# Performance work log

Measured on AMD Instinct MI355X. Metric: run time of the kernel, lower is better.

Reference implementation:

```python
import jax, jax.numpy as jnp
import numpy as np

EPS = 1e-6


def setup_inputs() -> dict:
    key = jax.random.key(0)
    k1, k2 = jax.random.split(key)
    T, B, D, n = 2048, 16, 1024, 64
    x = jax.random.normal(k1, (T, B, D), dtype=jnp.float32)
    S0 = jnp.zeros((B, n, n), dtype=jnp.float32)
    G0 = jnp.zeros((B, n, n), dtype=jnp.float32)
    # xavier-uniform-ish init for each n x D block of the fused projection
    limit = float(np.sqrt(6.0 / (n + D)))
    W_kvqm = jax.random.uniform(k2, (4 * n, D), dtype=jnp.float32, minval=-limit, maxval=limit)
    b_s_gate = jnp.full((n,), 2.0, dtype=jnp.float32)
    b_g_gate = jnp.full((n,), 2.5, dtype=jnp.float32)
    return {"x": x, "S0": S0, "G0": G0, "W_kvqm": W_kvqm,
            "b_s_gate": b_s_gate, "b_g_gate": b_g_gate}


def _e81_forward(x, S0, G0, W_kvqm, b_s_gate, b_g_gate):
    T, B, D = x.shape
    n = b_s_gate.shape[0]
    # Fused projection: [T, B, 4n]
    proj = jnp.einsum('tbd,nd->tbn', x, W_kvqm)
    k_all, v_all, q_all, m_all = jnp.split(proj, 4, axis=-1)

    bs = b_s_gate[None, :, None]  # broadcast over [B, n(row), n(col)]
    bg = b_g_gate[None, :, None]

    def step(carry, kvqm):
        S, G = carry
        k, v, q, m_vec = kvqm  # each [B, n]
        k_norm = k / (jnp.linalg.norm(k, axis=-1, keepdims=True) + EPS)
        m_norm = m_vec / (jnp.linalg.norm(m_vec, axis=-1, keepdims=True) + EPS)

        gate_S = jax.nn.sigmoid(G + bs)
        s_retrieved = jnp.einsum('bij,bj->bi', S, k_norm)
        s_delta = v - s_retrieved
        S = gate_S * S + jnp.einsum('bi,bj->bij', s_delta, k_norm)

        gate_G = jax.nn.sigmoid(S + bg)
        g_retrieved = jnp.einsum('bij,bj->bi', G, m_norm)
        g_delta = s_delta - g_retrieved
        G = gate_G * G + jnp.einsum('bi,bj->bij', g_delta, m_norm)

        Sq = jnp.einsum('bij,bj->bi', S, q)
        out = Sq * jax.nn.silu(Sq)  # self-gated output
        return (S, G), out

    (S, G), output = jax.lax.scan(step, (S0, G0), (k_all, v_all, q_all, m_all))
    return output, S, G


def reference(x, S0, G0, W_kvqm, b_s_gate, b_g_gate):
    return _e81_forward(x, S0, G0, W_kvqm, b_s_gate, b_g_gate)
```

## Files before the change

kernel.cpp:

```cpp
#include <hip/hip_runtime.h>
#include <hip/hip_bf16.h>

#define EPS 1e-6f

typedef float f32x4 __attribute__((ext_vector_type(4)));
typedef short bf16x8 __attribute__((ext_vector_type(8)));

__device__ __forceinline__ unsigned f2bf(float x) {
  __hip_bfloat16 h = __float2bfloat16(x);
  return *reinterpret_cast<unsigned short*>(&h);
}
__device__ __forceinline__ unsigned split_pack(float x) {
  unsigned hi = f2bf(x);
  unsigned short hs = (unsigned short)hi;
  float hif = __bfloat162float(*reinterpret_cast<__hip_bfloat16*>(&hs));
  unsigned lo = f2bf(x - hif);
  return (lo << 16) | hi;
}

union FragCast { unsigned u[4]; bf16x8 v; };

constexpr int GBM = 128, GBK = 32;

__global__ __launch_bounds__(512) void proj_gemm_mfma(
    const float* __restrict__ A,
    const float* __restrict__ Bw,
    float* __restrict__ C,
    int M, int K) {
  __shared__ unsigned As[GBM * GBK];
  __shared__ unsigned Bs[256 * GBK];

  const int tid  = threadIdx.x;
  const int lane = tid & 63;
  const int wid  = tid >> 6;
  const int m0   = blockIdx.x * GBM;
  const int wm   = (wid >> 2) * 64;
  const int wn   = (wid & 3) * 64;

  const int ar = tid >> 2, ak = (tid & 3) * 8;
  const int br = tid >> 1, bk = (tid & 1) * 16;

  f32x4 acc[4][4] = {};

  for (int k0 = 0; k0 < K; k0 += GBK) {
    {
      const float* src = &A[(size_t)(m0 + ar) * K + k0 + ak];
      float4 v0 = *(const float4*)(src);
      float4 v1 = *(const float4*)(src + 4);
      unsigned p0[4] = {split_pack(v0.x), split_pack(v0.y),
                        split_pack(v0.z), split_pack(v0.w)};
      unsigned p1[4] = {split_pack(v1.x), split_pack(v1.y),
                        split_pack(v1.z), split_pack(v1.w)};
      unsigned swz  = (unsigned)(ar & 7) << 4;
      char* base = (char*)As + ar * 128;
      *(uint4*)(base + (((unsigned)ak * 4) ^ swz))       = *(uint4*)p0;
      *(uint4*)(base + (((unsigned)(ak + 4) * 4) ^ swz)) = *(uint4*)p1;
    }
    {
      const float* src = &Bw[(size_t)br * K + k0 + bk];
      unsigned swz = (unsigned)(br & 7) << 4;
      char* base = (char*)Bs + br * 128;
#pragma unroll
      for (int q = 0; q < 4; ++q) {
        float4 v = *(const float4*)(src + q * 4);
        unsigned p[4] = {split_pack(v.x), split_pack(v.y),
                         split_pack(v.z), split_pack(v.w)};
        *(uint4*)(base + (((unsigned)(bk + q * 4) * 4) ^ swz)) = *(uint4*)p;
      }
    }
    __syncthreads();

    unsigned ah[4][4], al[4][4];
    const unsigned ko = ((unsigned)(lane >> 4)) * 16;
#pragma unroll
    for (int mf = 0; mf < 4; ++mf) {
      int r = wm + mf * 16 + (lane & 15);
      unsigned swz = (unsigned)(r & 7) << 4;
      char* base = (char*)As + r * 128;
      uint4 w0 = *(uint4*)(base + (ko ^ swz));
      uint4 w1 = *(uint4*)(base + ((64 + ko) ^ swz));
      ah[mf][0] = __builtin_amdgcn_perm(w0.y, w0.x, 0x05040100);
      al[mf][0] = __builtin_amdgcn_perm(w0.y, w0.x, 0x07060302);
      ah[mf][1] = __builtin_amdgcn_perm(w0.w, w0.z, 0x05040100);
      al[mf][1] = __builtin_amdgcn_perm(w0.w, w0.z, 0x07060302);
      ah[mf][2] = __builtin_amdgcn_perm(w1.y, w1.x, 0x05040100);
      al[mf][2] = __builtin_amdgcn_perm(w1.y, w1.x, 0x07060302);
      ah[mf][3] = __builtin_amdgcn_perm(w1.w, w1.z, 0x05040100);
      al[mf][3] = __builtin_amdgcn_perm(w1.w, w1.z, 0x07060302);
    }

#pragma unroll
    for (int nf = 0; nf < 4; ++nf) {
      int r = wn + nf * 16 + (lane & 15);
      unsigned swz = (unsigned)(r & 7) << 4;
      char* base = (char*)Bs + r * 128;
      uint4 w0 = *(uint4*)(base + (ko ^ swz));
      uint4 w1 = *(uint4*)(base + ((64 + ko) ^ swz));
      FragCast bh, bl;
      bh.u[0] = __builtin_amdgcn_perm(w0.y, w0.x, 0x05040100);
      bl.u[0] = __builtin_amdgcn_perm(w0.y, w0.x, 0x07060302);
      bh.u[1] = __builtin_amdgcn_perm(w0.w, w0.z, 0x05040100);
      bl.u[1] = __builtin_amdgcn_perm(w0.w, w0.z, 0x07060302);
      bh.u[2] = __builtin_amdgcn_perm(w1.y, w1.x, 0x05040100);
      bl.u[2] = __builtin_amdgcn_perm(w1.y, w1.x, 0x07060302);
      bh.u[3] = __builtin_amdgcn_perm(w1.w, w1.z, 0x05040100);
      bl.u[3] = __builtin_amdgcn_perm(w1.w, w1.z, 0x07060302);
#pragma unroll
      for (int mf = 0; mf < 4; ++mf) {
        FragCast fah, fal;
        fah.u[0] = ah[mf][0]; fah.u[1] = ah[mf][1];
        fah.u[2] = ah[mf][2]; fah.u[3] = ah[mf][3];
        fal.u[0] = al[mf][0]; fal.u[1] = al[mf][1];
        fal.u[2] = al[mf][2]; fal.u[3] = al[mf][3];
        acc[mf][nf] = __builtin_amdgcn_mfma_f32_16x16x32_bf16(
            fah.v, bh.v, acc[mf][nf], 0, 0, 0);
        acc[mf][nf] = __builtin_amdgcn_mfma_f32_16x16x32_bf16(
            fah.v, bl.v, acc[mf][nf], 0, 0, 0);
        acc[mf][nf] = __builtin_amdgcn_mfma_f32_16x16x32_bf16(
            fal.v, bh.v, acc[mf][nf], 0, 0, 0);
      }
    }
    __syncthreads();
  }

#pragma unroll
  for (int mf = 0; mf < 4; ++mf) {
    int row = m0 + wm + mf * 16 + (lane >> 4) * 4;
#pragma unroll
    for (int nf = 0; nf < 4; ++nf) {
      int col = wn + nf * 16 + (lane & 15);
#pragma unroll
      for (int r = 0; r < 4; ++r)
        C[(size_t)(row + r) * 256 + col] = acc[mf][nf][r];
    }
  }
}

template <int CTRL>
__device__ __forceinline__ float dpp_mov(float v) {
  return __int_as_float(
      __builtin_amdgcn_update_dpp(0, __float_as_int(v), CTRL, 0xF, 0xF, true));
}

__device__ __forceinline__ float wave_sum_all(float v) {
  v += dpp_mov<0x121>(v);
  v += dpp_mov<0x122>(v);
  v += dpp_mov<0x124>(v);
  v += dpp_mov<0x128>(v);
  v += dpp_mov<0x142>(v);
  v += dpp_mov<0x143>(v);
  return __int_as_float(__builtin_amdgcn_readlane(__float_as_int(v), 63));
}

__device__ __forceinline__ float reduce16(float v) {
  v += dpp_mov<0x121>(v);
  v += dpp_mov<0x122>(v);
  v += dpp_mov<0x124>(v);
  v += dpp_mov<0x128>(v);
  return v;
}

#define L2E 1.4426950408889634f
__device__ __forceinline__ float sigm_b(float x, float nb) {
  float t = __builtin_amdgcn_exp2f(fmaf(x, -L2E, nb));
  return __builtin_amdgcn_rcpf(1.0f + t);
}
__device__ __forceinline__ float sigm(float x) {
  float t = __builtin_amdgcn_exp2f(x * -L2E);
  return __builtin_amdgcn_rcpf(1.0f + t);
}

__global__ __launch_bounds__(256) void normalize_km(float* __restrict__ proj,
                                                    int rows) {
  const int w = blockIdx.x * 4 + (threadIdx.x >> 6);
  const int lane = threadIdx.x & 63;
  if (w >= rows) return;
  float* p = proj + (size_t)w * 256;
  const int src = 16 * (lane & 3) + (lane >> 2);
  float k = p[src];
  float q = p[128 + src];
  float m = p[192 + src];
  float nk = sqrtf(wave_sum_all(k * k)) + EPS;
  float nm = sqrtf(wave_sum_all(m * m)) + EPS;
  p[lane]       = k * __builtin_amdgcn_rcpf(nk);
  p[128 + lane] = q;
  p[192 + lane] = m * __builtin_amdgcn_rcpf(nm);
}

#define PSTR 4096

__global__ __launch_bounds__(64) void e81_scan(
    const float* __restrict__ proj,
    const float* __restrict__ S0,
    const float* __restrict__ G0,
    const float* __restrict__ bsg,
    const float* __restrict__ bgg,
    float* __restrict__ dout,
    int T) {
  const int lane = threadIdx.x;
  const int l = lane & 15;
  const int g = lane >> 4;
  const int b  = blockIdx.x >> 4;
  const int wb = blockIdx.x & 15;
  const int row = wb * 4 + g;

  const size_t sgbase = ((size_t)(b * 64 + row)) * 64 + l;
  float S[4], G[4];
#pragma unroll
  for (int e = 0; e < 4; ++e) {
    S[e] = S0[sgbase + 16 * e];
    G[e] = G0[sgbase + 16 * e];
  }
  const float nbs = -bsg[row] * L2E;
  const float nbg = -bgg[row] * L2E;

  float* outp = dout;
  float* Sout = dout + (size_t)T * 16 * 64;
  float* Gout = Sout + 16 * 64 * 64;

  const float* pA = proj + b * 256;
  const float* pB = pA + PSTR;
  float4 kA = *(const float4*)(pA + 4 * l);
  float4 qA = *(const float4*)(pA + 128 + 4 * l);
  float4 mA = *(const float4*)(pA + 192 + 4 * l);
  float  vA = pA[64 + row];
  float4 kB = *(const float4*)(pB + 4 * l);
  float4 qB = *(const float4*)(pB + 128 + 4 * l);
  float4 mB = *(const float4*)(pB + 192 + 4 * l);
  float  vB = pB[64 + row];

#define STEP(k_, q_, m_, v_, tidx)                                       \
  {                                                                      \
                     \
    float gs0 = sigm_b(G[0], nbs), gs1 = sigm_b(G[1], nbs);              \
    float gs2 = sigm_b(G[2], nbs), gs3 = sigm_b(G[3], nbs);              \
    float sr = S[0] * k_.x;                                              \
    sr = fmaf(S[1], k_.y, sr);                                           \
    sr = fmaf(S[2], k_.z, sr);                                           \
    sr = fmaf(S[3], k_.w, sr);                                           \
    sr = reduce16(sr);                                                   \
    float gr = G[0] * m_.x;                                              \
    gr = fmaf(G[1], m_.y, gr);                                           \
    gr = fmaf(G[2], m_.z, gr);                                           \
    gr = fmaf(G[3], m_.w, gr);                                           \
    gr = reduce16(gr);                                                   \
    float sdelta = v_ - sr;                                              \
    S[0] = fmaf(gs0, S[0], sdelta * k_.x);                               \
    S[1] = fmaf(gs1, S[1], sdelta * k_.y);                               \
    S[2] = fmaf(gs2, S[2], sdelta * k_.z);                               \
    S[3] = fmaf(gs3, S[3], sdelta * k_.w);                               \
     \
    float sq = S[0] * q_.x;                                              \
    sq = fmaf(S[1], q_.y, sq);                                           \
    sq = fmaf(S[2], q_.z, sq);                                           \
    sq = fmaf(S[3], q_.w, sq);                                           \
    sq = reduce16(sq);                                                   \
    float gd = sdelta - gr;                                              \
    G[0] = fmaf(sigm_b(S[0], nbg), G[0], gd * m_.x);                     \
    G[1] = fmaf(sigm_b(S[1], nbg), G[1], gd * m_.y);                     \
    G[2] = fmaf(sigm_b(S[2], nbg), G[2], gd * m_.z);                     \
    G[3] = fmaf(sigm_b(S[3], nbg), G[3], gd * m_.w);                     \
    if (l == 0) outp[(((size_t)(tidx) << 4) + b) * 64 + row] = sq;       \
  }

  for (int t = 0; t < T; t += 2) {
    const float* pA2 = (t + 2 < T) ? (pA + 2 * PSTR) : pA;
    const float* pB2 = (t + 3 < T) ? (pB + 2 * PSTR) : pB;
    float4 kA2 = *(const float4*)(pA2 + 4 * l);
    float4 qA2 = *(const float4*)(pA2 + 128 + 4 * l);
    float4 mA2 = *(const float4*)(pA2 + 192 + 4 * l);
    float  vA2 = pA2[64 + row];
    float4 kB2 = *(const float4*)(pB2 + 4 * l);
    float4 qB2 = *(const float4*)(pB2 + 128 + 4 * l);
    float4 mB2 = *(const float4*)(pB2 + 192 + 4 * l);
    float  vB2 = pB2[64 + row];

    STEP(kA, qA, mA, vA, t)
    STEP(kB, qB, mB, vB, t + 1)

    kA = kA2; qA = qA2; mA = mA2; vA = vA2; pA = pA2;
    kB = kB2; qB = qB2; mB = mB2; vB = vB2; pB = pB2;
  }
#undef STEP

#pragma unroll
  for (int e = 0; e < 4; ++e) {
    Sout[sgbase + 16 * e] = S[e];
    Gout[sgbase + 16 * e] = G[e];
  }
}

__global__ __launch_bounds__(256) void out_act(float* __restrict__ o, int n4) {
  int i = blockIdx.x * 256 + threadIdx.x;
  if (i < n4) {
    float4 x = *(float4*)(o + 4 * i);
    float4 r;
    r.x = x.x * x.x * sigm(x.x);
    r.y = x.y * x.y * sigm(x.y);
    r.z = x.z * x.z * sigm(x.z);
    r.w = x.w * x.w * sigm(x.w);
    *(float4*)(o + 4 * i) = r;
  }
}

extern "C" void kernel_launch(void* const* d_in, const int* in_sizes, int n_in,
                              void* d_out, int out_size, void* d_ws, size_t ws_size,
                              hipStream_t stream) {
  const float* x  = (const float*)d_in[0];
  const float* S0 = (const float*)d_in[1];
  const float* G0 = (const float*)d_in[2];
  const float* W  = (const float*)d_in[3];
  const float* bs = (const float*)d_in[4];
  const float* bg = (const float*)d_in[5];
  float* out = (float*)d_out;
  float* proj = (float*)d_ws;

  const int B = 16, D = 1024;
  const int T = in_sizes[0] / (B * D);
  const int M = T * B;

  proj_gemm_mfma<<<dim3(M / GBM), 512, 0, stream>>>(x, W, proj, M, D);

  normalize_km<<<dim3(M / 4), 256, 0, stream>>>(proj, M);

  e81_scan<<<dim3(256), 64, 0, stream>>>(proj, S0, G0, bs, bg, out, T);

  const int n4 = T * B * 64 / 4;
  out_act<<<dim3((n4 + 255) / 256), 256, 0, stream>>>(out, n4);
}
```

Before: 757.2 us.

## Fuse k/m normalization into GEMM epilogue and remap scan to one row per wave

Removes the separate normalize_km kernel by computing row L2 norms of the k and m column blocks inside the projection GEMM epilogue, then scaling the stored values there. The scan kernel is remapped so that each wave owns one state row, with one element per lane, and the block grows to 256 threads. Dot products then need 64-lane reductions, done with permlane swaps or a DPP fallback, where before each lane held 4 elements and a 16-lane reduction sufficed. The remap also drops the old column permutation of k and m in the projection buffer, so loads become plain per-lane scalars. The aim is to cut one kernel launch plus its memory pass, and to shorten per-lane serial work on the latency-bound recurrence, at the cost of longer cross-lane reductions.

After: 772.6 us. 2.0% more time.

```diff
diff --git a/kernel.cpp b/kernel.cpp
--- a/kernel.cpp
+++ b/kernel.cpp
@@ -2,9 +2,55 @@
 #include <hip/hip_bf16.h>
 
 #define EPS 1e-6f
+#define L2E 1.4426950408889634f
 
 typedef float f32x4 __attribute__((ext_vector_type(4)));
 typedef short bf16x8 __attribute__((ext_vector_type(8)));
+
+template <int CTRL>
+__device__ __forceinline__ float dpp_mov(float v) {
+  return __int_as_float(
+      __builtin_amdgcn_update_dpp(0, __float_as_int(v), CTRL, 0xF, 0xF, true));
+}
+
+__device__ __forceinline__ float reduce16(float v) {
+  v += dpp_mov<0x121>(v);
+  v += dpp_mov<0x122>(v);
+  v += dpp_mov<0x124>(v);
+  v += dpp_mov<0x128>(v);
+  return v;
+}
+
+__device__ __forceinline__ float reduce64_all(float v) {
+  v = reduce16(v);
+#if __has_builtin(__builtin_amdgcn_permlane16_swap) && \
+    __has_builtin(__builtin_amdgcn_permlane32_swap)
+  {
+    auto r = __builtin_amdgcn_permlane16_swap(__float_as_int(v),
+                                              __float_as_int(v), false, false);
+    v = __int_as_float(r[0]) + __int_as_float(r[1]);
+  }
+  {
+    auto r = __builtin_amdgcn_permlane32_swap(__float_as_int(v),
+                                              __float_as_int(v), false, false);
+    v = __int_as_float(r[0]) + __int_as_float(r[1]);
+  }
+  return v;
+#else
+  v += dpp_mov<0x142>(v);
+  v += dpp_mov<0x143>(v);
+  return __int_as_float(__builtin_amdgcn_readlane(__float_as_int(v), 63));
+#endif
+}
+
+__device__ __forceinline__ float sigm_b(float x, float nb) {
+  float t = __builtin_amdgcn_exp2f(fmaf(x, -L2E, nb));
+  return __builtin_amdgcn_rcpf(1.0f + t);
+}
+__device__ __forceinline__ float sigm(float x) {
+  float t = __builtin_amdgcn_exp2f(x * -L2E);
+  return __builtin_amdgcn_rcpf(1.0f + t);
+}
 
 __device__ __forceinline__ unsigned f2bf(float x) {
   __hip_bfloat16 h = __float2bfloat16(x);
@@ -123,6 +169,27 @@
     __syncthreads();
   }
 
+  float rn[4][4];
+  const int wcol = wid & 3;
+  if (wcol == 0 || wcol == 3) {
+#pragma unroll
+    for (int mf = 0; mf < 4; ++mf)
+#pragma unroll
+      for (int r = 0; r < 4; ++r) {
+        float ss = acc[mf][0][r] * acc[mf][0][r];
+        ss = fmaf(acc[mf][1][r], acc[mf][1][r], ss);
+        ss = fmaf(acc[mf][2][r], acc[mf][2][r], ss);
+        ss = fmaf(acc[mf][3][r], acc[mf][3][r], ss);
+        ss = reduce16(ss);
+        rn[mf][r] = __builtin_amdgcn_rcpf(sqrtf(ss) + EPS);
+      }
+  } else {
+#pragma unroll
+    for (int mf = 0; mf < 4; ++mf)
+#pragma unroll
+      for (int r = 0; r < 4; ++r) rn[mf][r] = 1.0f;
+  }
+
 #pragma unroll
   for (int mf = 0; mf < 4; ++mf) {
     int row = m0 + wm + mf * 16 + (lane >> 4) * 4;
@@ -131,65 +198,14 @@
       int col = wn + nf * 16 + (lane & 15);
 #pragma unroll
       for (int r = 0; r < 4; ++r)
-        C[(size_t)(row + r) * 256 + col] = acc[mf][nf][r];
-    }
-  }
-}
-
-template <int CTRL>
-__device__ __forceinline__ float dpp_mov(float v) {
-  return __int_as_float(
-      __builtin_amdgcn_update_dpp(0, __float_as_int(v), CTRL, 0xF, 0xF, true));
-}
-
-__device__ __forceinline__ float wave_sum_all(float v) {
-  v += dpp_mov<0x121>(v);
-  v += dpp_mov<0x122>(v);
-  v += dpp_mov<0x124>(v);
-  v += dpp_mov<0x128>(v);
-  v += dpp_mov<0x142>(v);
-  v += dpp_mov<0x143>(v);
-  return __int_as_float(__builtin_amdgcn_readlane(__float_as_int(v), 63));
-}
-
-__device__ __forceinline__ float reduce16(float v) {
-  v += dpp_mov<0x121>(v);
-  v += dpp_mov<0x122>(v);
-  v += dpp_mov<0x124>(v);
-  v += dpp_mov<0x128>(v);
-  return v;
-}
-
-#define L2E 1.4426950408889634f
-__device__ __forceinline__ float sigm_b(float x, float nb) {
-  float t = __builtin_amdgcn_exp2f(fmaf(x, -L2E, nb));
-  return __builtin_amdgcn_rcpf(1.0f + t);
-}
-__device__ __forceinline__ float sigm(float x) {
-  float t = __builtin_amdgcn_exp2f(x * -L2E);
-  return __builtin_amdgcn_rcpf(1.0f + t);
-}
-
-__global__ __launch_bounds__(256) void normalize_km(float* __restrict__ proj,
-                                                    int rows) {
-  const int w = blockIdx.x * 4 + (threadIdx.x >> 6);
-  const int lane = threadIdx.x & 63;
-  if (w >= rows) return;
-  float* p = proj + (size_t)w * 256;
-  const int src = 16 * (lane & 3) + (lane >> 2);
-  float k = p[src];
-  float q = p[128 + src];
-  float m = p[192 + src];
-  float nk = sqrtf(wave_sum_all(k * k)) + EPS;
-  float nm = sqrtf(wave_sum_all(m * m)) + EPS;
-  p[lane]       = k * __builtin_amdgcn_rcpf(nk);
-  p[128 + lane] = q;
-  p[192 + lane] = m * __builtin_amdgcn_rcpf(nm);
+        C[(size_t)(row + r) * 256 + col] = acc[mf][nf][r] * rn[mf][r];
+    }
+  }
 }
 
 #define PSTR 4096
 
-__global__ __launch_bounds__(64) void e81_scan(
+__global__ __launch_bounds__(256) void e81_scan(
     const float* __restrict__ proj,
     const float* __restrict__ S0,
     const float* __restrict__ G0,
@@ -197,20 +213,14 @@
     const float* __restrict__ bgg,
     float* __restrict__ dout,
     int T) {
-  const int lane = threadIdx.x;
-  const int l = lane & 15;
-  const int g = lane >> 4;
-  const int b  = blockIdx.x >> 4;
-  const int wb = blockIdx.x & 15;
-  const int row = wb * 4 + g;
-
-  const size_t sgbase = ((size_t)(b * 64 + row)) * 64 + l;
-  float S[4], G[4];
-#pragma unroll
-  for (int e = 0; e < 4; ++e) {
-    S[e] = S0[sgbase + 16 * e];
-    G[e] = G0[sgbase + 16 * e];
-  }
+  const int lane = threadIdx.x & 63;
+  const int wave = threadIdx.x >> 6;
+  const int b    = blockIdx.x >> 4;
+  const int row  = ((blockIdx.x & 15) << 2) + wave;
+
+  const size_t sgi = ((size_t)(b * 64 + row)) * 64 + lane;
+  float S = S0[sgi];
+  float G = G0[sgi];
   const float nbs = -bsg[row] * L2E;
   const float nbg = -bgg[row] * L2E;
 
@@ -220,60 +230,29 @@
 
   const float* pA = proj + b * 256;
   const float* pB = pA + PSTR;
-  float4 kA = *(const float4*)(pA + 4 * l);
-  float4 qA = *(const float4*)(pA + 128 + 4 * l);
-  float4 mA = *(const float4*)(pA + 192 + 4 * l);
-  float  vA = pA[64 + row];
-  float4 kB = *(const float4*)(pB + 4 * l);
-  float4 qB = *(const float4*)(pB + 128 + 4 * l);
-  float4 mB = *(const float4*)(pB + 192 + 4 * l);
-  float  vB = pB[64 + row];
-
-#define STEP(k_, q_, m_, v_, tidx)                                       \
-  {                                                                      \
-                     \
-    float gs0 = sigm_b(G[0], nbs), gs1 = sigm_b(G[1], nbs);              \
-    float gs2 = sigm_b(G[2], nbs), gs3 = sigm_b(G[3], nbs);              \
-    float sr = S[0] * k_.x;                                              \
-    sr = fmaf(S[1], k_.y, sr);                                           \
-    sr = fmaf(S[2], k_.z, sr);                                           \
-    sr = fmaf(S[3], k_.w, sr);                                           \
-    sr = reduce16(sr);                                                   \
-    float gr = G[0] * m_.x;                                              \
-    gr = fmaf(G[1], m_.y, gr);                                           \
-    gr = fmaf(G[2], m_.z, gr);                                           \
-    gr = fmaf(G[3], m_.w, gr);                                           \
-    gr = reduce16(gr);                                                   \
-    float sdelta = v_ - sr;                                              \
-    S[0] = fmaf(gs0, S[0], sdelta * k_.x);                               \
-    S[1] = fmaf(gs1, S[1], sdelta * k_.y);                               \
-    S[2] = fmaf(gs2, S[2], sdelta * k_.z);                               \
-    S[3] = fmaf(gs3, S[3], sdelta * k_.w);                               \
-     \
-    float sq = S[0] * q_.x;                                              \
-    sq = fmaf(S[1], q_.y, sq);                                           \
-    sq = fmaf(S[2], q_.z, sq);                                           \
-    sq = fmaf(S[3], q_.w, sq);                                           \
-    sq = reduce16(sq);                                                   \
-    float gd = sdelta - gr;                                              \
-    G[0] = fmaf(sigm_b(S[0], nbg), G[0], gd * m_.x);                     \
-    G[1] = fmaf(sigm_b(S[1], nbg), G[1], gd * m_.y);                     \
-    G[2] = fmaf(sigm_b(S[2], nbg), G[2], gd * m_.z);                     \
-    G[3] = fmaf(sigm_b(S[3], nbg), G[3], gd * m_.w);                     \
-    if (l == 0) outp[(((size_t)(tidx) << 4) + b) * 64 + row] = sq;       \
+  float kA = pA[lane], qA = pA[128 + lane], mA = pA[192 + lane], vA = pA[64 + row];
+  float kB = pB[lane], qB = pB[128 + lane], mB = pB[192 + lane], vB = pB[64 + row];
+
+#define STEP(k_, q_, m_, v_, tidx)                                   \
+  {                                                                  \
+    float gs = sigm_b(G, nbs);                \
+    float sr = reduce64_all(S * k_);                                 \
+    float gr = reduce64_all(G * m_);                                 \
+    float sdelta = v_ - sr;                                          \
+    S = fmaf(gs, S, sdelta * k_);                                    \
+    float sq = reduce64_all(S * q_);                                 \
+    float gg = sigm_b(S, nbg);                                       \
+    G = fmaf(gg, G, (sdelta - gr) * m_);                             \
+    if (lane == 0) outp[(((size_t)(tidx) << 4) + b) * 64 + row] = sq;\
   }
 
   for (int t = 0; t < T; t += 2) {
     const float* pA2 = (t + 2 < T) ? (pA + 2 * PSTR) : pA;
     const float* pB2 = (t + 3 < T) ? (pB + 2 * PSTR) : pB;
-    float4 kA2 = *(const float4*)(pA2 + 4 * l);
-    float4 qA2 = *(const float4*)(pA2 + 128 + 4 * l);
-    float4 mA2 = *(const float4*)(pA2 + 192 + 4 * l);
-    float  vA2 = pA2[64 + row];
-    float4 kB2 = *(const float4*)(pB2 + 4 * l);
-    float4 qB2 = *(const float4*)(pB2 + 128 + 4 * l);
-    float4 mB2 = *(const float4*)(pB2 + 192 + 4 * l);
-    float  vB2 = pB2[64 + row];
+    float kA2 = pA2[lane], qA2 = pA2[128 + lane], mA2 = pA2[192 + lane],
+          vA2 = pA2[64 + row];
+    float kB2 = pB2[lane], qB2 = pB2[128 + lane], mB2 = pB2[192 + lane],
+          vB2 = pB2[64 + row];
 
     STEP(kA, qA, mA, vA, t)
     STEP(kB, qB, mB, vB, t + 1)
@@ -283,11 +262,8 @@
   }
 #undef STEP
 
-#pragma unroll
-  for (int e = 0; e < 4; ++e) {
-    Sout[sgbase + 16 * e] = S[e];
-    Gout[sgbase + 16 * e] = G[e];
-  }
+  Sout[sgi] = S;
+  Gout[sgi] = G;
 }
 
 __global__ __launch_bounds__(256) void out_act(float* __restrict__ o, int n4) {
@@ -321,9 +297,7 @@
 
   proj_gemm_mfma<<<dim3(M / GBM), 512, 0, stream>>>(x, W, proj, M, D);
 
-  normalize_km<<<dim3(M / 4), 256, 0, stream>>>(proj, M);
-
-  e81_scan<<<dim3(256), 64, 0, stream>>>(proj, S0, G0, bs, bg, out, T);
+  e81_scan<<<dim3(256), 256, 0, stream>>>(proj, S0, G0, bs, bg, out, T);
 
   const int n4 = T * B * 64 / 4;
   out_act<<<dim3((n4 + 255) / 256), 256, 0, stream>>>(out, n4);
```
